# Performance work log

Hardware: AMD Instinct MI355X
Metric: run time of the kernel (lower is better)

The kernel has to match this reference:

```python
import jax, jax.numpy as jnp
import numpy as np

HEAD_SIZE = 64


def setup_inputs() -> dict:
    key = jax.random.key(0)
    k1, k2, k3, k4 = jax.random.split(key, 4)
    B, T, E = 8, 2048, 1024
    x = jax.random.normal(k1, (B, T, E), dtype=jnp.float32)
    # nn.Linear(n_embd, head_size, bias=False) weights: [head_size, n_embd]
    s = 1.0 / np.sqrt(E)
    Wk = jax.random.uniform(k2, (HEAD_SIZE, E), jnp.float32, -s, s)
    Wq = jax.random.uniform(k3, (HEAD_SIZE, E), jnp.float32, -s, s)
    Wv = jax.random.uniform(k4, (HEAD_SIZE, E), jnp.float32, -s, s)
    return {"x": x, "Wk": Wk, "Wq": Wq, "Wv": Wv}


def reference(x, Wk, Wq, Wv):
    # x: [B, T, E]; W*: [D, E] with D = head_size
    B, T, E = x.shape
    k = jnp.einsum("bte,de->btd", x, Wk)  # [B,T,D]
    q = jnp.einsum("bte,de->btd", x, Wq)
    v = jnp.einsum("bte,de->btd", x, Wv)
    scale = k.shape[-1] ** -0.5
    wei = jnp.einsum("btd,bsd->bts", q, k) * scale  # [B,T,T]
    causal = jnp.tril(jnp.ones((T, T), dtype=bool))
    wei = jnp.where(causal, wei, -jnp.inf)
    wei = jax.nn.softmax(wei, axis=-1)
    # dropout p=0.0 (eval): identity
    return jnp.einsum("bts,bsd->btd", wei, v)
```

## Files before the change

### kernel.cpp

```cpp
#include <hip/hip_runtime.h>
#include <hip/hip_bf16.h>


typedef __bf16 bf16x8 __attribute__((ext_vector_type(8)));
typedef float  f32x4  __attribute__((ext_vector_type(4)));

#define T_SEQ 2048
#define E_DIM 1024
#define D_HEAD 64
#define M_TOT 16384
#define NSPLIT 4
#define SC_LOG2E 0.18033688011112042f

__device__ __forceinline__ unsigned short f2b(float f) {
  union { float f; unsigned int u; } cv; cv.f = f;
  unsigned int u = cv.u;
  u += 0x7FFFu + ((u >> 16) & 1u);
  return (unsigned short)(u >> 16);
}

__device__ __forceinline__ unsigned int f2b2(float a, float b) {
#if __has_builtin(__builtin_amdgcn_cvt_pk_bf16_f32)
  typedef __bf16 bf16x2_t __attribute__((ext_vector_type(2)));
  union { bf16x2_t v; unsigned int u; } cv;
  cv.v = __builtin_amdgcn_cvt_pk_bf16_f32(a, b);
  return cv.u;
#else
  return (unsigned int)f2b(a) | ((unsigned int)f2b(b) << 16);
#endif
}

__device__ __forceinline__ void dma16(const unsigned short* g, unsigned short* l) {
  __builtin_amdgcn_global_load_lds(
      (const __attribute__((address_space(1))) void*)g,
      (__attribute__((address_space(3))) void*)l, 16, 0, 0);
}

__global__ __launch_bounds__(256) void wcvt_kernel(
    const float* __restrict__ Wk, const float* __restrict__ Wq,
    const float* __restrict__ Wv, unsigned short* __restrict__ Wb)
{
  int i = blockIdx.x * 256 + threadIdx.x;
  int n = i >> 8, c4 = i & 255;
  const float* src = (n < 64) ? Wq + n * E_DIM
                   : (n < 128) ? Wk + (n - 64) * E_DIM
                               : Wv + (n - 128) * E_DIM;
  float4 v = *(const float4*)(src + c4 * 4);
  *(uint2*)(Wb + (size_t)n * E_DIM + c4 * 4) = make_uint2(f2b2(v.x, v.y), f2b2(v.z, v.w));
}

__global__ __launch_bounds__(256, 2) void proj_kernel(
    const float* __restrict__ x, const unsigned short* __restrict__ Wb,
    unsigned short* __restrict__ qws, unsigned short* __restrict__ kws,
    unsigned short* __restrict__ vtws)
{
  __shared__ __align__(16) unsigned short x_lds[2][32 * 64];
  __shared__ __align__(16) unsigned short w_lds[2][192 * 64];

  const int tid = threadIdx.x, wv = tid >> 6, lane = tid & 63;
  const int c = lane & 15, quad = lane >> 4;
  const int row0 = blockIdx.x * 32;

  const int f0r = tid >> 4, f0c = tid & 15;
  const int f1r = 16 + f0r;
  const float* xp0 = x + (size_t)(row0 + f0r) * E_DIM + f0c * 4;
  const float* xp1 = x + (size_t)(row0 + f1r) * E_DIM + f0c * 4;
  const int xa0 = f0r * 64 + (((f0c >> 1) ^ (f0r & 7)) << 3) + (f0c & 1) * 4;
  const int xa1 = f1r * 64 + (((f0c >> 1) ^ (f1r & 7)) << 3) + (f0c & 1) * 4;

  auto stageW = [&](int k0, int buf) {
    for (int j = 0; j < 6; ++j) {
      int base_r = (wv * 6 + j) * 8;
      int r = base_r + (lane >> 3);
      int g = (lane & 7) ^ (r & 7);
      dma16(Wb + (size_t)r * E_DIM + k0 + g * 8, &w_lds[buf][base_r * 64]);
    }
  };
  auto writeX = [&](float4 v0, float4 v1, int buf) {
    *(uint2*)&x_lds[buf][xa0] = make_uint2(f2b2(v0.x, v0.y), f2b2(v0.z, v0.w));
    *(uint2*)&x_lds[buf][xa1] = make_uint2(f2b2(v1.x, v1.y), f2b2(v1.z, v1.w));
  };

  f32x4 acc[6];
  for (int j = 0; j < 6; ++j)
    for (int r = 0; r < 4; ++r) acc[j][r] = 0.0f;

  stageW(0, 0);
  {
    float4 v0 = *(const float4*)xp0;
    float4 v1 = *(const float4*)xp1;
    writeX(v0, v1, 0);
  }

  for (int s = 0; s < 16; ++s) {
    const int cur = s & 1;
    __syncthreads();
    float4 v0, v1;
    if (s < 15) {
      const int k1 = (s + 1) * 64;
      stageW(k1, cur ^ 1);
      v0 = *(const float4*)(xp0 + k1);
      v1 = *(const float4*)(xp1 + k1);
    }
    for (int ks = 0; ks < 2; ++ks) {
      const int pg = ((ks * 4 + quad) ^ (c & 7)) << 3;
      bf16x8 a0 = *(const bf16x8*)&x_lds[cur][c * 64 + pg];
      bf16x8 a1 = *(const bf16x8*)&x_lds[cur][(16 + c) * 64 + pg];
      for (int j = 0; j < 3; ++j) {
        const int n = (wv * 3 + j) * 16 + c;
        bf16x8 bb = *(const bf16x8*)&w_lds[cur][n * 64 + pg];
        acc[j * 2]     = __builtin_amdgcn_mfma_f32_16x16x32_bf16(a0, bb, acc[j * 2], 0, 0, 0);
        acc[j * 2 + 1] = __builtin_amdgcn_mfma_f32_16x16x32_bf16(a1, bb, acc[j * 2 + 1], 0, 0, 0);
      }
    }
    if (s < 15) writeX(v0, v1, cur ^ 1);
  }

  for (int mt = 0; mt < 2; ++mt) {
    const int rbase = row0 + mt * 16 + quad * 4;
    for (int j = 0; j < 3; ++j) {
      const int nt = wv * 3 + j;
      const f32x4 a = acc[j * 2 + mt];
      if (nt < 4) {
        int d = nt * 16 + c;
        for (int r = 0; r < 4; ++r)
          qws[(size_t)(rbase + r) * D_HEAD + d] = f2b(a[r] * SC_LOG2E);
      } else if (nt < 8) {
        int d = (nt - 4) * 16 + c;
        for (int r = 0; r < 4; ++r)
          kws[(size_t)(rbase + r) * D_HEAD + d] = f2b(a[r]);
      } else {
        int d = (nt - 8) * 16 + c;
        int bb = rbase >> 11, tt = rbase & 2047;
        *(ushort4*)&vtws[(size_t)bb * D_HEAD * T_SEQ + (size_t)d * T_SEQ + tt] =
            make_ushort4(f2b(a[0]), f2b(a[1]), f2b(a[2]), f2b(a[3]));
      }
    }
  }
}

__global__ __launch_bounds__(256, 4) void attn_kernel(
    const unsigned short* __restrict__ qws, const unsigned short* __restrict__ kws,
    const unsigned short* __restrict__ vtws,
    unsigned short* __restrict__ opart, float* __restrict__ lpart)
{
  __shared__ __align__(16) unsigned short k_lds[2 * 64 * 64];
  __shared__ __align__(16) unsigned short v_lds[2 * 64 * 64];
  __shared__ __align__(16) unsigned short p_lds[64 * 64];

  const int tid = threadIdx.x, wv = tid >> 6, lane = tid & 63;
  const int c = lane & 15, quad = lane >> 4;
  const int qt = blockIdx.x, b = blockIdx.y, sg = blockIdx.z;
  const int t0 = qt * 64;
  const size_t qkb = (size_t)b * T_SEQ * D_HEAD;
  const size_t vtb = (size_t)b * D_HEAD * T_SEQ;
  const int niter = (qt >= sg) ? ((qt - sg) >> 2) + 1 : 0;
  const int rloc = wv * 16 + quad * 4;
  const size_t prow = ((size_t)sg * 8 + b) * T_SEQ;

  if (niter == 0) {
    for (int nt = 0; nt < 4; ++nt)
      for (int r = 0; r < 4; ++r)
        opart[(prow + t0 + rloc + r) * D_HEAD + nt * 16 + c] = 0;
    if (c == 0)
      for (int r = 0; r < 4; ++r) lpart[prow + t0 + rloc + r] = 0.0f;
    return;
  }

  const int mrow = wv * 16 + c;
  const bf16x8 qf0 = *(const bf16x8*)(qws + qkb + (size_t)(t0 + mrow) * D_HEAD + quad * 8);
  const bf16x8 qf1 = *(const bf16x8*)(qws + qkb + (size_t)(t0 + mrow) * D_HEAD + 32 + quad * 8);

  bf16x8 ones;
  { union { unsigned short s[8]; bf16x8 v; } o;
    for (int i = 0; i < 8; ++i) o.s[i] = 0x3F80;
    ones = o.v; }

  f32x4 acc_o[4], acc_l;
  for (int r = 0; r < 4; ++r) acc_l[r] = 0.0f;
  for (int nt = 0; nt < 4; ++nt)
    for (int r = 0; r < 4; ++r) acc_o[nt][r] = 0.0f;

  auto stageKV = [&](int s0, int buf) {
    unsigned short* kb = k_lds + buf * 4096;
    unsigned short* vb = v_lds + buf * 4096;
    for (int j = 0; j < 2; ++j) {
      int base = (wv * 2 + j) * 64;
      int p = base + lane;
      int r = p >> 3, g = (p & 7) ^ (r & 7);
      dma16(kws + qkb + (size_t)(s0 + r) * D_HEAD + g * 8, kb + base * 8);
    }
    for (int j = 0; j < 2; ++j) {
      int base = (wv * 2 + j) * 64;
      int p = base + lane;
      int r = p >> 3, g = (p & 7) ^ (r & 7);
      dma16(vtws + vtb + (size_t)r * T_SEQ + s0 + g * 8, vb + base * 8);
    }
  };

  const bool mydiag = (sg == (qt & 3));
  stageKV(sg * 64, 0);

  for (int it = 0; it < niter; ++it) {
    const int s0 = (sg + 4 * it) * 64;
    const int cur = it & 1;
    __syncthreads();
    if (it + 1 < niter) stageKV((sg + 4 * (it + 1)) * 64, cur ^ 1);

    const unsigned short* kb = k_lds + cur * 4096;
    const unsigned short* vb = v_lds + cur * 4096;

    f32x4 accs[4];
    for (int nt = 0; nt < 4; ++nt)
      for (int r = 0; r < 4; ++r) accs[nt][r] = 0.0f;
    for (int nt = 0; nt < 4; ++nt) {
      int n = nt * 16 + c;
      bf16x8 kf0 = *(const bf16x8*)&kb[n * 64 + ((quad ^ (n & 7)) << 3)];
      bf16x8 kf1 = *(const bf16x8*)&kb[n * 64 + (((4 + quad) ^ (n & 7)) << 3)];
      accs[nt] = __builtin_amdgcn_mfma_f32_16x16x32_bf16(qf0, kf0, accs[nt], 0, 0, 0);
      accs[nt] = __builtin_amdgcn_mfma_f32_16x16x32_bf16(qf1, kf1, accs[nt], 0, 0, 0);
    }
    if (mydiag && it == niter - 1) {
      for (int nt = 0; nt < 4; ++nt) {
        int scol = s0 + nt * 16 + c;
        for (int r = 0; r < 4; ++r)
          if (scol > t0 + rloc + r) accs[nt][r] = -__builtin_inff();
      }
    }

    for (int nt = 0; nt < 4; ++nt)
      for (int r = 0; r < 4; ++r)
        accs[nt][r] = __builtin_exp2f(accs[nt][r]);

    for (int nt = 0; nt < 4; ++nt)
      for (int r = 0; r < 4; ++r) {
        int rr = rloc + r;
        p_lds[rr * 64 + (((nt * 2 + (c >> 3)) ^ (rr & 7)) << 3) + (c & 7)] = f2b(accs[nt][r]);
      }

    for (int ks = 0; ks < 2; ++ks) {
      int kg = ks * 4 + quad;
      bf16x8 pf = *(const bf16x8*)&p_lds[mrow * 64 + ((kg ^ (mrow & 7)) << 3)];
      acc_l = __builtin_amdgcn_mfma_f32_16x16x32_bf16(pf, ones, acc_l, 0, 0, 0);
      for (int nt = 0; nt < 4; ++nt) {
        int n = nt * 16 + c;
        bf16x8 vv = *(const bf16x8*)&vb[n * 64 + ((kg ^ (n & 7)) << 3)];
        acc_o[nt] = __builtin_amdgcn_mfma_f32_16x16x32_bf16(pf, vv, acc_o[nt], 0, 0, 0);
      }
    }
  }

  for (int nt = 0; nt < 4; ++nt)
    for (int r = 0; r < 4; ++r)
      opart[(prow + t0 + rloc + r) * D_HEAD + nt * 16 + c] = f2b(acc_o[nt][r]);
  if (c == 0)
    for (int r = 0; r < 4; ++r) lpart[prow + t0 + rloc + r] = acc_l[r];
}

__global__ __launch_bounds__(256) void merge_kernel(
    const unsigned short* __restrict__ opart, const float* __restrict__ lpart,
    float* __restrict__ out)
{
  int gid = blockIdx.x * 256 + threadIdx.x;
  int gr = gid >> 4, d4 = (gid & 15) * 4;
  float L = 0.0f;
  for (int i = 0; i < NSPLIT; ++i) L += lpart[(size_t)i * M_TOT + gr];
  float inv = 1.0f / L;
  float4 o = make_float4(0.f, 0.f, 0.f, 0.f);
  for (int i = 0; i < NSPLIT; ++i) {
    ushort4 u = *(const ushort4*)(opart + (size_t)i * M_TOT * D_HEAD + (size_t)gr * D_HEAD + d4);
    union { unsigned int u; float f; } cx, cy, cz, cw;
    cx.u = (unsigned int)u.x << 16; cy.u = (unsigned int)u.y << 16;
    cz.u = (unsigned int)u.z << 16; cw.u = (unsigned int)u.w << 16;
    o.x += cx.f; o.y += cy.f; o.z += cz.f; o.w += cw.f;
  }
  o.x *= inv; o.y *= inv; o.z *= inv; o.w *= inv;
  *(float4*)(out + (size_t)gr * D_HEAD + d4) = o;
}

extern "C" void kernel_launch(void* const* d_in, const int* in_sizes, int n_in,
                              void* d_out, int out_size, void* d_ws, size_t ws_size,
                              hipStream_t stream) {
  const float* x  = (const float*)d_in[0];
  const float* Wk = (const float*)d_in[1];
  const float* Wq = (const float*)d_in[2];
  const float* Wv = (const float*)d_in[3];
  float* out = (float*)d_out;

  unsigned short* qws   = (unsigned short*)d_ws;
  unsigned short* kws   = qws + (size_t)M_TOT * D_HEAD;
  unsigned short* vtws  = kws + (size_t)M_TOT * D_HEAD;
  unsigned short* Wb    = vtws + (size_t)M_TOT * D_HEAD;
  unsigned short* opart = Wb + 192 * E_DIM;
  float* lpart = (float*)(opart + (size_t)NSPLIT * M_TOT * D_HEAD);

  wcvt_kernel<<<192, 256, 0, stream>>>(Wk, Wq, Wv, Wb);
  proj_kernel<<<M_TOT / 32, 256, 0, stream>>>(x, Wb, qws, kws, vtws);
  attn_kernel<<<dim3(T_SEQ / 64, 8, NSPLIT), 256, 0, stream>>>(qws, kws, vtws, opart, lpart);
  merge_kernel<<<M_TOT * 16 / 256, 256, 0, stream>>>(opart, lpart, out);
}
```

Measured before the change: 139.3 us.

## Load K/V fragments directly from global in MFMA-ready layout, smaller attention blocks

The projection kernel now writes K and V into fragment-friendly layouts: K split into two 32-wide halves per row, and V tiled in 32-token blocks. The attention kernel then loads MFMA operands straight from global memory into registers, dropping LDS staging, double buffering and the per-iteration block barrier. Blocks shrink to 128 threads covering 32 query rows and are issued in reverse order so the longest causal rows start first. Empty split blocks now exit without writing, and the merge kernel skips splits beyond the causal limit. In exchange, every wave re-reads K/V from global or L2 with no reuse across waves, and it relies on cache hits to hide latency.

New measurement: 226.6 us. 1.63x slower.

```diff
diff --git a/kernel.cpp b/kernel.cpp
--- a/kernel.cpp
+++ b/kernel.cpp
@@ -30,7 +30,7 @@
 #endif
 }
 
-__device__ __forceinline__ void dma16(const unsigned short* g, unsigned short* l) {
+__device__ __forceinline__ void dma16(const void* g, void* l) {
   __builtin_amdgcn_global_load_lds(
       (const __attribute__((address_space(1))) void*)g,
       (__attribute__((address_space(3))) void*)l, 16, 0, 0);
@@ -51,8 +51,8 @@
 
 __global__ __launch_bounds__(256, 2) void proj_kernel(
     const float* __restrict__ x, const unsigned short* __restrict__ Wb,
-    unsigned short* __restrict__ qws, unsigned short* __restrict__ kws,
-    unsigned short* __restrict__ vtws)
+    unsigned short* __restrict__ qws, unsigned short* __restrict__ kfws,
+    unsigned short* __restrict__ vfws)
 {
   __shared__ __align__(16) unsigned short x_lds[2][32 * 64];
   __shared__ __align__(16) unsigned short w_lds[2][192 * 64];
@@ -60,6 +60,7 @@
   const int tid = threadIdx.x, wv = tid >> 6, lane = tid & 63;
   const int c = lane & 15, quad = lane >> 4;
   const int row0 = blockIdx.x * 32;
+  const int b = row0 >> 11, tloc = row0 & 2047;
 
   const int f0r = tid >> 4, f0c = tid & 15;
   const int f1r = 16 + f0r;
@@ -117,55 +118,48 @@
   }
 
   for (int mt = 0; mt < 2; ++mt) {
-    const int rbase = row0 + mt * 16 + quad * 4;
+    const int rg = row0 + mt * 16 + quad * 4;
+    const int sl = tloc + mt * 16 + quad * 4;
     for (int j = 0; j < 3; ++j) {
       const int nt = wv * 3 + j;
       const f32x4 a = acc[j * 2 + mt];
       if (nt < 4) {
         int d = nt * 16 + c;
         for (int r = 0; r < 4; ++r)
-          qws[(size_t)(rbase + r) * D_HEAD + d] = f2b(a[r] * SC_LOG2E);
+          qws[(size_t)(rg + r) * D_HEAD + d] = f2b(a[r] * SC_LOG2E);
       } else if (nt < 8) {
         int d = (nt - 4) * 16 + c;
+        size_t base = ((size_t)(b * 2 + (d >> 5)) * T_SEQ + sl) * 32 + (d & 31);
         for (int r = 0; r < 4; ++r)
-          kws[(size_t)(rbase + r) * D_HEAD + d] = f2b(a[r]);
+          kfws[base + (size_t)r * 32] = f2b(a[r]);
       } else {
         int d = (nt - 8) * 16 + c;
-        int bb = rbase >> 11, tt = rbase & 2047;
-        *(ushort4*)&vtws[(size_t)bb * D_HEAD * T_SEQ + (size_t)d * T_SEQ + tt] =
+        size_t base = ((size_t)(b * 64 + (sl >> 5)) * 64 + d) * 32 + (sl & 31);
+        *(ushort4*)&vfws[base] =
             make_ushort4(f2b(a[0]), f2b(a[1]), f2b(a[2]), f2b(a[3]));
       }
     }
   }
 }
 
-__global__ __launch_bounds__(256, 4) void attn_kernel(
-    const unsigned short* __restrict__ qws, const unsigned short* __restrict__ kws,
-    const unsigned short* __restrict__ vtws,
+__global__ __launch_bounds__(128, 8) void attn_kernel(
+    const unsigned short* __restrict__ qws, const unsigned short* __restrict__ kfws,
+    const unsigned short* __restrict__ vfws,
     unsigned short* __restrict__ opart, float* __restrict__ lpart)
 {
-  __shared__ __align__(16) unsigned short k_lds[2 * 64 * 64];
-  __shared__ __align__(16) unsigned short v_lds[2 * 64 * 64];
-  __shared__ __align__(16) unsigned short p_lds[64 * 64];
+  __shared__ __align__(16) unsigned short p_lds[32 * 64];
 
   const int tid = threadIdx.x, wv = tid >> 6, lane = tid & 63;
   const int c = lane & 15, quad = lane >> 4;
-  const int qt = blockIdx.x, b = blockIdx.y, sg = blockIdx.z;
-  const int t0 = qt * 64;
+  const int qt32 = 63 - blockIdx.x, b = blockIdx.y, sg = blockIdx.z;
+  const int t0 = qt32 * 32;
+  const int jmaxq = qt32 >> 1;
+  const int niter = (jmaxq >= sg) ? ((jmaxq - sg) >> 2) + 1 : 0;
+  if (niter == 0) return;
+
   const size_t qkb = (size_t)b * T_SEQ * D_HEAD;
-  const size_t vtb = (size_t)b * D_HEAD * T_SEQ;
-  const int niter = (qt >= sg) ? ((qt - sg) >> 2) + 1 : 0;
   const int rloc = wv * 16 + quad * 4;
   const size_t prow = ((size_t)sg * 8 + b) * T_SEQ;
-
-  if (niter == 0) {
-    for (int nt = 0; nt < 4; ++nt)
-      for (int r = 0; r < 4; ++r)
-        opart[(prow + t0 + rloc + r) * D_HEAD + nt * 16 + c] = 0;
-    if (c == 0)
-      for (int r = 0; r < 4; ++r) lpart[prow + t0 + rloc + r] = 0.0f;
-    return;
-  }
 
   const int mrow = wv * 16 + c;
   const bf16x8 qf0 = *(const bf16x8*)(qws + qkb + (size_t)(t0 + mrow) * D_HEAD + quad * 8);
@@ -181,44 +175,30 @@
   for (int nt = 0; nt < 4; ++nt)
     for (int r = 0; r < 4; ++r) acc_o[nt][r] = 0.0f;
 
-  auto stageKV = [&](int s0, int buf) {
-    unsigned short* kb = k_lds + buf * 4096;
-    unsigned short* vb = v_lds + buf * 4096;
-    for (int j = 0; j < 2; ++j) {
-      int base = (wv * 2 + j) * 64;
-      int p = base + lane;
-      int r = p >> 3, g = (p & 7) ^ (r & 7);
-      dma16(kws + qkb + (size_t)(s0 + r) * D_HEAD + g * 8, kb + base * 8);
-    }
-    for (int j = 0; j < 2; ++j) {
-      int base = (wv * 2 + j) * 64;
-      int p = base + lane;
-      int r = p >> 3, g = (p & 7) ^ (r & 7);
-      dma16(vtws + vtb + (size_t)r * T_SEQ + s0 + g * 8, vb + base * 8);
-    }
-  };
-
-  const bool mydiag = (sg == (qt & 3));
-  stageKV(sg * 64, 0);
+  const unsigned short* Kb = kfws + (size_t)b * 2 * T_SEQ * 32;
+  const unsigned short* Vb = vfws + (size_t)b * 64 * D_HEAD * 32;
+  const bool mydiag = (sg == (jmaxq & 3));
 
   for (int it = 0; it < niter; ++it) {
     const int s0 = (sg + 4 * it) * 64;
-    const int cur = it & 1;
-    __syncthreads();
-    if (it + 1 < niter) stageKV((sg + 4 * (it + 1)) * 64, cur ^ 1);
-
-    const unsigned short* kb = k_lds + cur * 4096;
-    const unsigned short* vb = v_lds + cur * 4096;
+
+    bf16x8 vf[8];
+    for (int ks = 0; ks < 2; ++ks) {
+      int sb = (s0 >> 5) + ks;
+      for (int nt = 0; nt < 4; ++nt)
+        vf[ks * 4 + nt] = *(const bf16x8*)(Vb + ((size_t)sb * 64 + nt * 16 + c) * 32 + quad * 8);
+    }
+    bf16x8 kf[8];
+    for (int nt = 0; nt < 4; ++nt)
+      for (int kb = 0; kb < 2; ++kb)
+        kf[nt * 2 + kb] = *(const bf16x8*)(Kb + ((size_t)kb * T_SEQ + s0 + nt * 16 + c) * 32 + quad * 8);
 
     f32x4 accs[4];
     for (int nt = 0; nt < 4; ++nt)
       for (int r = 0; r < 4; ++r) accs[nt][r] = 0.0f;
     for (int nt = 0; nt < 4; ++nt) {
-      int n = nt * 16 + c;
-      bf16x8 kf0 = *(const bf16x8*)&kb[n * 64 + ((quad ^ (n & 7)) << 3)];
-      bf16x8 kf1 = *(const bf16x8*)&kb[n * 64 + (((4 + quad) ^ (n & 7)) << 3)];
-      accs[nt] = __builtin_amdgcn_mfma_f32_16x16x32_bf16(qf0, kf0, accs[nt], 0, 0, 0);
-      accs[nt] = __builtin_amdgcn_mfma_f32_16x16x32_bf16(qf1, kf1, accs[nt], 0, 0, 0);
+      accs[nt] = __builtin_amdgcn_mfma_f32_16x16x32_bf16(qf0, kf[nt * 2], accs[nt], 0, 0, 0);
+      accs[nt] = __builtin_amdgcn_mfma_f32_16x16x32_bf16(qf1, kf[nt * 2 + 1], accs[nt], 0, 0, 0);
     }
     if (mydiag && it == niter - 1) {
       for (int nt = 0; nt < 4; ++nt) {
@@ -242,11 +222,8 @@
       int kg = ks * 4 + quad;
       bf16x8 pf = *(const bf16x8*)&p_lds[mrow * 64 + ((kg ^ (mrow & 7)) << 3)];
       acc_l = __builtin_amdgcn_mfma_f32_16x16x32_bf16(pf, ones, acc_l, 0, 0, 0);
-      for (int nt = 0; nt < 4; ++nt) {
-        int n = nt * 16 + c;
-        bf16x8 vv = *(const bf16x8*)&vb[n * 64 + ((kg ^ (n & 7)) << 3)];
-        acc_o[nt] = __builtin_amdgcn_mfma_f32_16x16x32_bf16(pf, vv, acc_o[nt], 0, 0, 0);
-      }
+      for (int nt = 0; nt < 4; ++nt)
+        acc_o[nt] = __builtin_amdgcn_mfma_f32_16x16x32_bf16(pf, vf[ks * 4 + nt], acc_o[nt], 0, 0, 0);
     }
   }
 
@@ -263,17 +240,19 @@
 {
   int gid = blockIdx.x * 256 + threadIdx.x;
   int gr = gid >> 4, d4 = (gid & 15) * 4;
+  const int jmax = (gr & 2047) >> 6;
   float L = 0.0f;
-  for (int i = 0; i < NSPLIT; ++i) L += lpart[(size_t)i * M_TOT + gr];
-  float inv = 1.0f / L;
   float4 o = make_float4(0.f, 0.f, 0.f, 0.f);
   for (int i = 0; i < NSPLIT; ++i) {
+    if (i > jmax) break;
+    L += lpart[(size_t)i * M_TOT + gr];
     ushort4 u = *(const ushort4*)(opart + (size_t)i * M_TOT * D_HEAD + (size_t)gr * D_HEAD + d4);
     union { unsigned int u; float f; } cx, cy, cz, cw;
     cx.u = (unsigned int)u.x << 16; cy.u = (unsigned int)u.y << 16;
     cz.u = (unsigned int)u.z << 16; cw.u = (unsigned int)u.w << 16;
     o.x += cx.f; o.y += cy.f; o.z += cz.f; o.w += cw.f;
   }
+  float inv = 1.0f / L;
   o.x *= inv; o.y *= inv; o.z *= inv; o.w *= inv;
   *(float4*)(out + (size_t)gr * D_HEAD + d4) = o;
 }
@@ -288,14 +267,14 @@
   float* out = (float*)d_out;
 
   unsigned short* qws   = (unsigned short*)d_ws;
-  unsigned short* kws   = qws + (size_t)M_TOT * D_HEAD;
-  unsigned short* vtws  = kws + (size_t)M_TOT * D_HEAD;
-  unsigned short* Wb    = vtws + (size_t)M_TOT * D_HEAD;
+  unsigned short* kfws  = qws + (size_t)M_TOT * D_HEAD;
+  unsigned short* vfws  = kfws + (size_t)M_TOT * D_HEAD;
+  unsigned short* Wb    = vfws + (size_t)M_TOT * D_HEAD;
   unsigned short* opart = Wb + 192 * E_DIM;
   float* lpart = (float*)(opart + (size_t)NSPLIT * M_TOT * D_HEAD);
 
   wcvt_kernel<<<192, 256, 0, stream>>>(Wk, Wq, Wv, Wb);
-  proj_kernel<<<M_TOT / 32, 256, 0, stream>>>(x, Wb, qws, kws, vtws);
-  attn_kernel<<<dim3(T_SEQ / 64, 8, NSPLIT), 256, 0, stream>>>(qws, kws, vtws, opart, lpart);
+  proj_kernel<<<M_TOT / 32, 256, 0, stream>>>(x, Wb, qws, kfws, vfws);
+  attn_kernel<<<dim3(64, 8, NSPLIT), 128, 0, stream>>>(qws, kfws, vfws, opart, lpart);
   merge_kernel<<<M_TOT * 16 / 256, 256, 0, stream>>>(opart, lpart, out);
 }
```
